# Performance work log

Hardware: AMD Instinct MI355X
Metric: run time of the kernel (lower is better)

The kernel has to match this reference:

```python
import jax, jax.numpy as jnp
import numpy as np

DIM = 512

def setup_inputs() -> dict:
    key = jax.random.key(0)
    ks = jax.random.split(key, 10)
    B, N, D = 8, 4096, DIM
    s = 1.0 / np.sqrt(D)
    return {
        "x": jax.random.normal(ks[0], (B, N, D), dtype=jnp.float32),
        "wq": jax.random.normal(ks[1], (D, D), dtype=jnp.float32) * s,
        "bq": jnp.zeros((D,), dtype=jnp.float32),
        "wk": jax.random.normal(ks[2], (D, D), dtype=jnp.float32) * s,
        "bk": jnp.zeros((D,), dtype=jnp.float32),
        "wp": jax.random.normal(ks[3], (D, D), dtype=jnp.float32) * s,
        "bp": jnp.zeros((D,), dtype=jnp.float32),
        "wf": jax.random.normal(ks[4], (D, D), dtype=jnp.float32) * s,
        "bf": jnp.zeros((D,), dtype=jnp.float32),
        "w_g": jax.random.normal(ks[5], (D, 1), dtype=jnp.float32),
    }

def reference(x, wq, bq, wk, bk, wp, bp, wf, bf, w_g):
    D = x.shape[-1]
    scale = D ** (-0.5)
    query = x @ wq + bq                      # [B,N,D]
    key_t = x @ wk + bk                      # [B,N,D]
    # l2 normalize along last dim (tf.math.l2_normalize uses eps=1e-12 via rsqrt of max(sum_sq, eps))
    def l2n(t):
        ss = jnp.sum(t * t, axis=-1, keepdims=True)
        return t * jax.lax.rsqrt(jnp.maximum(ss, 1e-12))
    query = l2n(query)
    key_t = l2n(key_t)
    query_weight = query @ w_g               # [B,N,1]
    scaled = query_weight * scale
    # Faithful to TF code: softmax over axis=-1 of a size-1 axis -> all ones
    attn = jax.nn.softmax(scaled, axis=-1)   # [B,N,1] == 1.0
    global_queries = jnp.sum(attn * query, axis=1)  # [B,D]
    gq = global_queries[:, None, :]          # broadcast over N (tile)
    out = (gq * key_t) @ wp + bp + query     # [B,N,D]
    out = out @ wf + bf
    return out
```

## Files before the change

### kernel.cpp

```cpp
#include <hip/hip_runtime.h>
#include <stdint.h>

typedef __bf16 bf16x8 __attribute__((ext_vector_type(8)));
typedef float floatx4 __attribute__((ext_vector_type(4)));
typedef unsigned short u16;
typedef u16 u16x8 __attribute__((ext_vector_type(8)));

__device__ __forceinline__ float bf2f(u16 u) {
    union { uint32_t i; float f; } v; v.i = ((uint32_t)u) << 16; return v.f;
}
__device__ __forceinline__ u16 f2bf(float f) {
    union { float f; uint32_t i; } v; v.f = f;
    uint32_t r = v.i + 0x7fffu + ((v.i >> 16) & 1u);
    return (u16)(r >> 16);
}

__device__ __forceinline__ void gload_lds16(const u16* g, u16* l) {
    __builtin_amdgcn_global_load_lds(
        (const __attribute__((address_space(1))) void*)g,
        (__attribute__((address_space(3))) void*)l,
        16, 0, 0);
}

#define BK 64
template<int EPI>
__global__ __launch_bounds__(512, 2) void gemm_bt(
    const u16* __restrict__ A, int lda,
    const u16* __restrict__ Bt, long bstride,
    const float* __restrict__ bias,
    const u16* __restrict__ addsrc, int ldadd,
    const float* __restrict__ ssq_add,
    const float* __restrict__ ssq_row,
    float* __restrict__ ssq_out,
    u16* __restrict__ C16, float* __restrict__ C32, int ldc,
    int K)
{
    __shared__ __attribute__((aligned(16))) u16 lds[2 * 32768];
    const int tid  = threadIdx.x;
    const int wave = tid >> 6;
    const int lane = tid & 63;
    const int quad = lane >> 4;
    const int l16  = lane & 15;
    const int wm = wave >> 2, wn = wave & 3;

    const int gx   = gridDim.x;
    const int nwg  = gx * gridDim.y;
    const int wgid = blockIdx.y * gx + blockIdx.x;
    const int cpx  = nwg >> 3;
    const int swz  = (wgid & 7) * cpx + (wgid >> 3);
    const int row0 = (swz / gx) * 256;
    const int col0 = (swz % gx) * 256;
    const int batch = row0 >> 12;
    const int Mtot  = gridDim.y * 256;

    floatx4 acc[8][4] = {};

    const int rsub = lane >> 3;
    const int ksub = ((lane & 7) ^ rsub) << 3;
    const u16* aptr[4]; const u16* bptr[4];
    const u16* Bb = Bt + (size_t)batch * bstride;
#pragma unroll
    for (int c = 0; c < 4; ++c) {
        const int cc = wave * 4 + c;
        aptr[c] = A  + (size_t)(row0 + cc * 8 + rsub) * lda + ksub;
        bptr[c] = Bb + (size_t)(col0 + cc * 8 + rsub) * K   + ksub;
    }

    const int NT = K >> 6;

#define STAGE(T, B)                                                        \
    {                                                                      \
        u16* sA_ = &lds[(B) * 32768];                                      \
        u16* sB_ = sA_ + 16384;                                            \
        const int kt_ = (T) * BK;                                          \
        _Pragma("unroll")                                                  \
        for (int c = 0; c < 4; ++c) {                                      \
            const int cc = wave * 4 + c;                                   \
            gload_lds16(aptr[c] + kt_, &sA_[cc * 512]);                    \
            gload_lds16(bptr[c] + kt_, &sB_[cc * 512]);                    \
        }                                                                  \
    }

    STAGE(0, 0);
    STAGE(1, 1);

    for (int t = 0; t < NT; ++t) {
        if (t + 1 < NT) asm volatile("s_waitcnt vmcnt(8)" ::: "memory");
        else            asm volatile("s_waitcnt vmcnt(0)" ::: "memory");
        __builtin_amdgcn_s_barrier();
        __builtin_amdgcn_sched_barrier(0);

        const u16* sA = &lds[(t & 1) * 32768];
        const u16* sB = sA + 16384;
#pragma unroll
        for (int ks = 0; ks < 2; ++ks) {
            const int cidx = ks * 4 + quad;
            const int pgo = ((cidx ^ (l16 & 7)) << 3);
            bf16x8 bfr[4];
#pragma unroll
            for (int n = 0; n < 4; ++n)
                bfr[n] = *(const bf16x8*)&sB[(wn * 64 + n * 16 + l16) * BK + pgo];
            __builtin_amdgcn_s_setprio(1);
#pragma unroll
            for (int m = 0; m < 8; ++m) {
                bf16x8 af = *(const bf16x8*)&sA[(wm * 128 + m * 16 + l16) * BK + pgo];
#pragma unroll
                for (int n = 0; n < 4; ++n)
                    acc[m][n] = __builtin_amdgcn_mfma_f32_16x16x32_bf16(af, bfr[n], acc[m][n], 0, 0, 0);
            }
            __builtin_amdgcn_s_setprio(0);
        }

        __builtin_amdgcn_sched_barrier(0);
        asm volatile("" ::: "memory");
        __builtin_amdgcn_s_barrier();
        asm volatile("" ::: "memory");
        if (t + 2 < NT) STAGE(t + 2, t & 1);
    }
#undef STAGE

    if constexpr (EPI == 0 || EPI == 1) {
        u16* til = lds;
#pragma unroll
        for (int h = 0; h < 2; ++h) {
            __syncthreads();
            if (wm == h) {
                float bv[4];
#pragma unroll
                for (int n = 0; n < 4; ++n) bv[n] = bias[col0 + wn * 64 + n * 16 + l16];
#pragma unroll
                for (int m = 0; m < 8; ++m) {
                    int rowl = m * 16 + quad * 4;
                    int rowb = row0 + h * 128 + rowl;
                    float rsr4[4], rsa4[4];
                    if constexpr (EPI == 1) {
                        float4 rr = *(const float4*)&ssq_row[rowb];
                        float4 ra = *(const float4*)&ssq_add[rowb];
                        rsr4[0] = rsqrtf(fmaxf(rr.x, 1e-12f));
                        rsr4[1] = rsqrtf(fmaxf(rr.y, 1e-12f));
                        rsr4[2] = rsqrtf(fmaxf(rr.z, 1e-12f));
                        rsr4[3] = rsqrtf(fmaxf(rr.w, 1e-12f));
                        rsa4[0] = rsqrtf(fmaxf(ra.x, 1e-12f));
                        rsa4[1] = rsqrtf(fmaxf(ra.y, 1e-12f));
                        rsa4[2] = rsqrtf(fmaxf(ra.z, 1e-12f));
                        rsa4[3] = rsqrtf(fmaxf(ra.w, 1e-12f));
                    }
#pragma unroll
                    for (int n = 0; n < 4; ++n) {
                        int tcol = wn * 64 + n * 16 + l16;
#pragma unroll
                        for (int t = 0; t < 4; ++t) {
                            float v;
                            if constexpr (EPI == 1) {
                                v = acc[m][n][t] * rsr4[t] + bv[n]
                                  + bf2f(addsrc[(size_t)(rowb + t) * ldadd + col0 + tcol]) * rsa4[t];
                            } else {
                                v = acc[m][n][t] + bv[n];
                            }
                            til[(rowl + t) * 264 + tcol] = f2bf(v);
                        }
                    }
                }
            }
            __syncthreads();
            float ssl[8];
#pragma unroll
            for (int c = 0; c < 8; ++c) {
                int r  = c * 16 + (tid >> 5);
                int cu = (tid & 31) * 8;
                ushort4 lo = *(const ushort4*)&til[r * 264 + cu];
                ushort4 hi = *(const ushort4*)&til[r * 264 + cu + 4];
                u16x8 o;
                o[0] = lo.x; o[1] = lo.y; o[2] = lo.z; o[3] = lo.w;
                o[4] = hi.x; o[5] = hi.y; o[6] = hi.z; o[7] = hi.w;
                *(u16x8*)&C16[(size_t)(row0 + h * 128 + r) * ldc + col0 + cu] = o;
                if constexpr (EPI == 0) {
                    float ss = 0.f;
#pragma unroll
                    for (int q2 = 0; q2 < 8; ++q2) { float f = bf2f(o[q2]); ss += f * f; }
                    ssl[c] = ss;
                }
            }
            if constexpr (EPI == 0) {
                float* so = ssq_out + (size_t)(col0 >> 9) * Mtot + row0 + h * 128;
#pragma unroll
                for (int c = 0; c < 8; ++c) {
                    float s = ssl[c];
                    s += __shfl_xor(s, 1);
                    s += __shfl_xor(s, 2);
                    s += __shfl_xor(s, 4);
                    s += __shfl_xor(s, 8);
                    s += __shfl_xor(s, 16);
                    if ((lane & 31) == 0) atomicAdd(&so[c * 16 + (tid >> 5)], s);
                }
            }
        }
    } else {
        float* ftile = (float*)lds;
#pragma unroll
        for (int p = 0; p < 4; ++p) {
            __syncthreads();
            if (wm == (p >> 1)) {
                float bv[4];
#pragma unroll
                for (int n = 0; n < 4; ++n) bv[n] = bias[col0 + wn * 64 + n * 16 + l16];
#pragma unroll
                for (int mi = 0; mi < 4; ++mi) {
                    int m = (p & 1) * 4 + mi;
                    int rowl = mi * 16 + quad * 4;
#pragma unroll
                    for (int n = 0; n < 4; ++n) {
                        int tcol = wn * 64 + n * 16 + l16;
#pragma unroll
                        for (int t = 0; t < 4; ++t)
                            ftile[(rowl + t) * 264 + tcol] = acc[m][n][t] + bv[n];
                    }
                }
            }
            __syncthreads();
#pragma unroll
            for (int c = 0; c < 8; ++c) {
                int r  = c * 8 + wave;
                int cu = lane * 4;
                float4 v = *(const float4*)&ftile[r * 264 + cu];
                *(float4*)&C32[(size_t)(row0 + p * 64 + r) * ldc + col0 + cu] = v;
            }
        }
    }
}

__global__ __launch_bounds__(256) void gsum_kernel(const u16* __restrict__ QK,
                                                   const float* __restrict__ ssqQ,
                                                   float* __restrict__ g)
{
    __shared__ float gtile[4][512];
    const int lane = threadIdx.x & 63;
    const int wave = threadIdx.x >> 6;
    const int row0 = blockIdx.x * 128 + wave * 32;
    const int batch = row0 >> 12;
    const int d = lane * 8;
    float gacc[8] = {};
    for (int rr = 0; rr < 32; ++rr) {
        int row = row0 + rr;
        float s = rsqrtf(fmaxf(ssqQ[row], 1e-12f));
        u16x8 q = *(const u16x8*)(QK + (size_t)row * 1024 + d);
#pragma unroll
        for (int i = 0; i < 8; ++i) gacc[i] += s * bf2f(q[i]);
    }
#pragma unroll
    for (int i = 0; i < 8; ++i) gtile[wave][d + i] = gacc[i];
    __syncthreads();
    int c2 = threadIdx.x * 2;
    float s0 = gtile[0][c2]     + gtile[1][c2]     + gtile[2][c2]     + gtile[3][c2];
    float s1 = gtile[0][c2 + 1] + gtile[1][c2 + 1] + gtile[2][c2 + 1] + gtile[3][c2 + 1];
    atomicAdd(&g[batch * 512 + c2], s0);
    atomicAdd(&g[batch * 512 + c2 + 1], s1);
}

__global__ __launch_bounds__(256) void scale_wp_kernel(const float* __restrict__ wp,
                                                       const float* __restrict__ g,
                                                       u16* __restrict__ BtP8)
{
    __shared__ u16 tile[32][34];
    const int b   = blockIdx.x >> 8;
    const int bid = blockIdx.x & 255;
    const int tk = bid & 15;
    const int tn = bid >> 4;
    const int c  = threadIdx.x & 31;
    const int r0 = threadIdx.x >> 5;
    const float* gb = g + b * 512;
#pragma unroll
    for (int i = 0; i < 4; ++i) {
        int r = r0 + i * 8;
        int k = tk * 32 + r;
        tile[r][c] = f2bf(gb[k] * wp[(size_t)k * 512 + tn * 32 + c]);
    }
    __syncthreads();
    u16* Bt = BtP8 + (size_t)b * 512 * 512;
#pragma unroll
    for (int i = 0; i < 4; ++i) {
        int r = r0 + i * 8;
        Bt[(size_t)(tn * 32 + r) * 512 + tk * 32 + c] = tile[c][r];
    }
}

__global__ __launch_bounds__(256) void convert_x_kernel(const float* __restrict__ x, u16* __restrict__ xb)
{
    size_t i = ((size_t)blockIdx.x * 256 + threadIdx.x) * 4;
    float4 v = *(const float4*)(x + i);
    ushort4 o;
    o.x = f2bf(v.x); o.y = f2bf(v.y); o.z = f2bf(v.z); o.w = f2bf(v.w);
    *(ushort4*)(xb + i) = o;
}

__global__ __launch_bounds__(256) void transpose3_kernel(
    const float* __restrict__ w0, const float* __restrict__ w1, const float* __restrict__ w2,
    u16* __restrict__ d0, u16* __restrict__ d1, u16* __restrict__ d2)
{
    __shared__ u16 tile[32][34];
    const int which = blockIdx.x >> 8;
    const float* W = (which == 0) ? w0 : (which == 1) ? w1 : w2;
    u16* Bt = (which == 0) ? d0 : (which == 1) ? d1 : d2;
    const int bid = blockIdx.x & 255;
    const int tk = bid & 15;
    const int tn = bid >> 4;
    const int c  = threadIdx.x & 31;
    const int r0 = threadIdx.x >> 5;
#pragma unroll
    for (int i = 0; i < 4; ++i) {
        int r = r0 + i * 8;
        tile[r][c] = f2bf(W[(size_t)(tk * 32 + r) * 512 + tn * 32 + c]);
    }
    __syncthreads();
#pragma unroll
    for (int i = 0; i < 4; ++i) {
        int r = r0 + i * 8;
        Bt[(size_t)(tn * 32 + r) * 512 + tk * 32 + c] = tile[c][r];
    }
}

__global__ __launch_bounds__(256) void setup_kernel(const float* __restrict__ bq,
                                                    const float* __restrict__ bk,
                                                    float* __restrict__ biasQK,
                                                    float* __restrict__ g,
                                                    float* __restrict__ ssq)
{
    int id = blockIdx.x * 256 + threadIdx.x;
    if (id < 1024) biasQK[id] = (id < 512) ? bq[id] : bk[id - 512];
    if (id < 4096) g[id] = 0.f;
    ssq[id] = 0.f;
}

extern "C" void kernel_launch(void* const* d_in, const int* in_sizes, int n_in,
                              void* d_out, int out_size, void* d_ws, size_t ws_size,
                              hipStream_t stream)
{
    const float* x  = (const float*)d_in[0];
    const float* wq = (const float*)d_in[1];
    const float* bq = (const float*)d_in[2];
    const float* wk = (const float*)d_in[3];
    const float* bk = (const float*)d_in[4];
    const float* wp = (const float*)d_in[5];
    const float* bp = (const float*)d_in[6];
    const float* wf = (const float*)d_in[7];
    const float* bf = (const float*)d_in[8];

    char* ws = (char*)d_ws;
    u16*   xb     = (u16*)(ws);
    u16*   T      = (u16*)(ws);
    u16*   QK     = (u16*)(ws + 33554432);
    u16*   Bt1    = (u16*)(ws + 100663296);
    u16*   BtP8   = (u16*)(ws + 101711872);
    u16*   BtF    = (u16*)(ws + 105906176);
    float* biasQK = (float*)(ws + 106430464);
    float* g      = (float*)(ws + 106434560);
    float* ssq    = (float*)(ws + 106450944);

    setup_kernel<<<256, 256, 0, stream>>>(bq, bk, biasQK, g, ssq);
    convert_x_kernel<<<16384, 256, 0, stream>>>(x, xb);
    transpose3_kernel<<<768, 256, 0, stream>>>(wq, wk, wf, Bt1, Bt1 + 512 * 512, BtF);

    gemm_bt<0><<<dim3(4, 128), 512, 0, stream>>>(
        xb, 512, Bt1, 0, biasQK, nullptr, 0, nullptr, nullptr, ssq, QK, nullptr, 1024, 512);
    gsum_kernel<<<256, 256, 0, stream>>>(QK, ssq, g);
    scale_wp_kernel<<<2048, 256, 0, stream>>>(wp, g, BtP8);
    gemm_bt<1><<<dim3(2, 128), 512, 0, stream>>>(
        QK + 512, 1024, BtP8, 512 * 512, bp, QK, 1024, ssq, ssq + 32768, nullptr, T, nullptr, 512, 512);
    gemm_bt<2><<<dim3(2, 128), 512, 0, stream>>>(
        T, 512, BtF, 0, bf, nullptr, 0, nullptr, nullptr, nullptr, nullptr, (float*)d_out, 512, 512);
}
```

Baseline: 254.8 us.

## Restructure GEMM main loop into four barrier-synchronized MFMA sub-phases with single-stage prefetch

The mainloop is rewritten so each K-tile is computed in four quadrant sub-phases. Each wave loads a quarter of its A/B fragments from LDS, synchronizes with a workgroup barrier, then issues a batch of MFMAs at raised priority, which staggers LDS reads and matrix work across waves. Global-to-LDS staging now prefetches one tile ahead instead of two, and the staging layout is regrouped by half-tile rows. The added barriers per tile and the shallower prefetch trade latency hiding for tighter inter-wave scheduling.

Result: no change. 257.3 us (+1.0%).

```diff
diff --git a/kernel.cpp b/kernel.cpp
--- a/kernel.cpp
+++ b/kernel.cpp
@@ -57,65 +57,133 @@
 
     const int rsub = lane >> 3;
     const int ksub = ((lane & 7) ^ rsub) << 3;
-    const u16* aptr[4]; const u16* bptr[4];
     const u16* Bb = Bt + (size_t)batch * bstride;
-#pragma unroll
-    for (int c = 0; c < 4; ++c) {
-        const int cc = wave * 4 + c;
-        aptr[c] = A  + (size_t)(row0 + cc * 8 + rsub) * lda + ksub;
-        bptr[c] = Bb + (size_t)(col0 + cc * 8 + rsub) * K   + ksub;
-    }
+    const u16* aP = A  + (size_t)(row0 + wave * 8 + rsub) * lda + ksub;
+    const u16* bP = Bb + (size_t)(col0 + wave * 8 + rsub) * K   + ksub;
 
     const int NT = K >> 6;
 
-#define STAGE(T, B)                                                        \
-    {                                                                      \
-        u16* sA_ = &lds[(B) * 32768];                                      \
-        u16* sB_ = sA_ + 16384;                                            \
-        const int kt_ = (T) * BK;                                          \
-        _Pragma("unroll")                                                  \
-        for (int c = 0; c < 4; ++c) {                                      \
-            const int cc = wave * 4 + c;                                   \
-            gload_lds16(aptr[c] + kt_, &sA_[cc * 512]);                    \
-            gload_lds16(bptr[c] + kt_, &sB_[cc * 512]);                    \
-        }                                                                  \
-    }
-
-    STAGE(0, 0);
-    STAGE(1, 1);
+#define STAGE(T)                                                              \
+    {                                                                         \
+        u16* dst_ = &lds[((T) & 1) * 32768];                                  \
+        const int kt_ = (T) * BK;                                             \
+        _Pragma("unroll")                                                     \
+        for (int h_ = 0; h_ < 2; ++h_)                                        \
+        { _Pragma("unroll")                                                   \
+          for (int j_ = 0; j_ < 2; ++j_) {                                    \
+            gload_lds16(aP + (size_t)(h_ * 128 + j_ * 64) * lda + kt_,        \
+                        dst_ + h_ * 8192 + j_ * 4096 + wave * 512);           \
+            gload_lds16(bP + (size_t)(h_ * 128 + j_ * 64) * K + kt_,          \
+                        dst_ + 16384 + h_ * 8192 + j_ * 4096 + wave * 512);   \
+          } }                                                                 \
+    }
+
+    STAGE(0);
+    asm volatile("s_waitcnt vmcnt(0)" ::: "memory");
+    __builtin_amdgcn_s_barrier();
 
     for (int t = 0; t < NT; ++t) {
-        if (t + 1 < NT) asm volatile("s_waitcnt vmcnt(8)" ::: "memory");
-        else            asm volatile("s_waitcnt vmcnt(0)" ::: "memory");
-        __builtin_amdgcn_s_barrier();
-        __builtin_amdgcn_sched_barrier(0);
-
-        const u16* sA = &lds[(t & 1) * 32768];
-        const u16* sB = sA + 16384;
-#pragma unroll
-        for (int ks = 0; ks < 2; ++ks) {
-            const int cidx = ks * 4 + quad;
-            const int pgo = ((cidx ^ (l16 & 7)) << 3);
-            bf16x8 bfr[4];
-#pragma unroll
-            for (int n = 0; n < 4; ++n)
-                bfr[n] = *(const bf16x8*)&sB[(wn * 64 + n * 16 + l16) * BK + pgo];
-            __builtin_amdgcn_s_setprio(1);
-#pragma unroll
-            for (int m = 0; m < 8; ++m) {
-                bf16x8 af = *(const bf16x8*)&sA[(wm * 128 + m * 16 + l16) * BK + pgo];
-#pragma unroll
-                for (int n = 0; n < 4; ++n)
-                    acc[m][n] = __builtin_amdgcn_mfma_f32_16x16x32_bf16(af, bfr[n], acc[m][n], 0, 0, 0);
-            }
-            __builtin_amdgcn_s_setprio(0);
-        }
-
-        __builtin_amdgcn_sched_barrier(0);
-        asm volatile("" ::: "memory");
-        __builtin_amdgcn_s_barrier();
-        asm volatile("" ::: "memory");
-        if (t + 2 < NT) STAGE(t + 2, t & 1);
+        const u16* buf = &lds[(t & 1) * 32768];
+        const u16* sA = buf + wm * 8192;
+        const u16* sB = buf + 16384 + (wn >> 1) * 8192;
+        const int brl = (wn & 1) * 64;
+        bf16x8 af[4][2], bb[2][2];
+
+#pragma unroll
+        for (int m = 0; m < 4; ++m)
+#pragma unroll
+            for (int ks = 0; ks < 2; ++ks)
+                af[m][ks] = *(const bf16x8*)&sA[(m * 16 + l16) * 64 + (((ks * 4 + quad) ^ (l16 & 7)) << 3)];
+#pragma unroll
+        for (int n = 0; n < 2; ++n)
+#pragma unroll
+            for (int ks = 0; ks < 2; ++ks)
+                bb[n][ks] = *(const bf16x8*)&sB[(brl + n * 16 + l16) * 64 + (((ks * 4 + quad) ^ (l16 & 7)) << 3)];
+        if (t + 1 < NT) STAGE(t + 1);
+        __builtin_amdgcn_sched_barrier(0);
+        __builtin_amdgcn_s_barrier();
+        asm volatile("s_waitcnt lgkmcnt(0)" ::: "memory");
+        __builtin_amdgcn_sched_barrier(0);
+        __builtin_amdgcn_s_setprio(1);
+#pragma unroll
+        for (int ks = 0; ks < 2; ++ks)
+#pragma unroll
+            for (int m = 0; m < 4; ++m)
+#pragma unroll
+                for (int n = 0; n < 2; ++n)
+                    acc[m][n] = __builtin_amdgcn_mfma_f32_16x16x32_bf16(af[m][ks], bb[n][ks], acc[m][n], 0, 0, 0);
+        __builtin_amdgcn_s_setprio(0);
+        __builtin_amdgcn_sched_barrier(0);
+        __builtin_amdgcn_s_barrier();
+
+#pragma unroll
+        for (int n = 0; n < 2; ++n)
+#pragma unroll
+            for (int ks = 0; ks < 2; ++ks)
+                bb[n][ks] = *(const bf16x8*)&sB[(brl + (n + 2) * 16 + l16) * 64 + (((ks * 4 + quad) ^ (l16 & 7)) << 3)];
+        __builtin_amdgcn_sched_barrier(0);
+        __builtin_amdgcn_s_barrier();
+        asm volatile("s_waitcnt lgkmcnt(0)" ::: "memory");
+        __builtin_amdgcn_sched_barrier(0);
+        __builtin_amdgcn_s_setprio(1);
+#pragma unroll
+        for (int ks = 0; ks < 2; ++ks)
+#pragma unroll
+            for (int m = 0; m < 4; ++m)
+#pragma unroll
+                for (int n = 0; n < 2; ++n)
+                    acc[m][n + 2] = __builtin_amdgcn_mfma_f32_16x16x32_bf16(af[m][ks], bb[n][ks], acc[m][n + 2], 0, 0, 0);
+        __builtin_amdgcn_s_setprio(0);
+        __builtin_amdgcn_sched_barrier(0);
+        __builtin_amdgcn_s_barrier();
+
+#pragma unroll
+        for (int m = 0; m < 4; ++m)
+#pragma unroll
+            for (int ks = 0; ks < 2; ++ks)
+                af[m][ks] = *(const bf16x8*)&sA[((m + 4) * 16 + l16) * 64 + (((ks * 4 + quad) ^ (l16 & 7)) << 3)];
+#pragma unroll
+        for (int n = 0; n < 2; ++n)
+#pragma unroll
+            for (int ks = 0; ks < 2; ++ks)
+                bb[n][ks] = *(const bf16x8*)&sB[(brl + n * 16 + l16) * 64 + (((ks * 4 + quad) ^ (l16 & 7)) << 3)];
+        __builtin_amdgcn_sched_barrier(0);
+        __builtin_amdgcn_s_barrier();
+        asm volatile("s_waitcnt lgkmcnt(0)" ::: "memory");
+        __builtin_amdgcn_sched_barrier(0);
+        __builtin_amdgcn_s_setprio(1);
+#pragma unroll
+        for (int ks = 0; ks < 2; ++ks)
+#pragma unroll
+            for (int m = 0; m < 4; ++m)
+#pragma unroll
+                for (int n = 0; n < 2; ++n)
+                    acc[m + 4][n] = __builtin_amdgcn_mfma_f32_16x16x32_bf16(af[m][ks], bb[n][ks], acc[m + 4][n], 0, 0, 0);
+        __builtin_amdgcn_s_setprio(0);
+        __builtin_amdgcn_sched_barrier(0);
+        __builtin_amdgcn_s_barrier();
+
+#pragma unroll
+        for (int n = 0; n < 2; ++n)
+#pragma unroll
+            for (int ks = 0; ks < 2; ++ks)
+                bb[n][ks] = *(const bf16x8*)&sB[(brl + (n + 2) * 16 + l16) * 64 + (((ks * 4 + quad) ^ (l16 & 7)) << 3)];
+        __builtin_amdgcn_sched_barrier(0);
+        __builtin_amdgcn_s_barrier();
+        asm volatile("s_waitcnt lgkmcnt(0)" ::: "memory");
+        __builtin_amdgcn_sched_barrier(0);
+        __builtin_amdgcn_s_setprio(1);
+#pragma unroll
+        for (int ks = 0; ks < 2; ++ks)
+#pragma unroll
+            for (int m = 0; m < 4; ++m)
+#pragma unroll
+                for (int n = 0; n < 2; ++n)
+                    acc[m + 4][n + 2] = __builtin_amdgcn_mfma_f32_16x16x32_bf16(af[m][ks], bb[n][ks], acc[m + 4][n + 2], 0, 0, 0);
+        __builtin_amdgcn_s_setprio(0);
+        __builtin_amdgcn_sched_barrier(0);
+        if (t + 1 < NT) asm volatile("s_waitcnt vmcnt(0)" ::: "memory");
+        __builtin_amdgcn_s_barrier();
     }
 #undef STAGE
 
```

## Fold projection and final GEMMs into one K=1024 GEMM via precomputed Wp·Wf

Applied to the files above, without the earlier changes.

Precomputes Wp@Wf (transposed, bf16) and the combined bias bp@Wf+bf once, then scales it per batch by the global query vector. The last two chained GEMMs become a single GEMM over the concatenated [query|key] activations (K=1024). The query half is rescaled mid-loop by the ratio of the two norm factors so a single key-norm scale can be applied in the epilogue. This removes the intermediate T round trip and one full 32K×512 GEMM pass, at the cost of extra small setup kernels and a different bf16 rounding order.

Result: no change. 256.0 us (+0.5%).

```diff
diff --git a/kernel.cpp b/kernel.cpp
--- a/kernel.cpp
+++ b/kernel.cpp
@@ -23,17 +23,149 @@
 }
 
 #define BK 64
-template<int EPI>
-__global__ __launch_bounds__(512, 2) void gemm_bt(
-    const u16* __restrict__ A, int lda,
-    const u16* __restrict__ Bt, long bstride,
+
+__global__ __launch_bounds__(512, 2) void gemm1_kernel(
+    const u16* __restrict__ A,
+    const u16* __restrict__ Bt,
     const float* __restrict__ bias,
-    const u16* __restrict__ addsrc, int ldadd,
-    const float* __restrict__ ssq_add,
-    const float* __restrict__ ssq_row,
     float* __restrict__ ssq_out,
-    u16* __restrict__ C16, float* __restrict__ C32, int ldc,
-    int K)
+    u16* __restrict__ C16)
+{
+    __shared__ __attribute__((aligned(16))) u16 lds[2 * 32768];
+    const int tid  = threadIdx.x;
+    const int wave = tid >> 6;
+    const int lane = tid & 63;
+    const int quad = lane >> 4;
+    const int l16  = lane & 15;
+    const int wm = wave >> 2, wn = wave & 3;
+
+    const int gx   = gridDim.x;
+    const int nwg  = gx * gridDim.y;
+    const int wgid = blockIdx.y * gx + blockIdx.x;
+    const int cpx  = nwg >> 3;
+    const int swz  = (wgid & 7) * cpx + (wgid >> 3);
+    const int row0 = (swz / gx) * 256;
+    const int col0 = (swz % gx) * 256;
+
+    floatx4 acc[8][4] = {};
+
+    const int rsub = lane >> 3;
+    const int ksub = ((lane & 7) ^ rsub) << 3;
+    const u16* aptr[4]; const u16* bptr[4];
+#pragma unroll
+    for (int c = 0; c < 4; ++c) {
+        const int cc = wave * 4 + c;
+        aptr[c] = A  + (size_t)(row0 + cc * 8 + rsub) * 512 + ksub;
+        bptr[c] = Bt + (size_t)(col0 + cc * 8 + rsub) * 512 + ksub;
+    }
+    const int NT = 8;
+
+#define STAGE1(T, B)                                                          \
+    {                                                                         \
+        u16* dA_ = &lds[(B) * 32768];                                         \
+        u16* dB_ = dA_ + 16384;                                               \
+        const int kt_ = (T) * BK;                                             \
+        _Pragma("unroll")                                                     \
+        for (int c = 0; c < 4; ++c) {                                         \
+            const int cc = wave * 4 + c;                                      \
+            gload_lds16(aptr[c] + kt_, dA_ + cc * 512);                       \
+            gload_lds16(bptr[c] + kt_, dB_ + cc * 512);                       \
+        }                                                                     \
+    }
+
+    STAGE1(0, 0);
+    STAGE1(1, 1);
+    for (int t = 0; t < NT; ++t) {
+        if (t + 1 < NT) asm volatile("s_waitcnt vmcnt(8)" ::: "memory");
+        else            asm volatile("s_waitcnt vmcnt(0)" ::: "memory");
+        __builtin_amdgcn_s_barrier();
+        __builtin_amdgcn_sched_barrier(0);
+        const u16* sA = &lds[(t & 1) * 32768];
+        const u16* sB = sA + 16384;
+#pragma unroll
+        for (int ks = 0; ks < 2; ++ks) {
+            const int pgo = (((ks * 4 + quad) ^ (l16 & 7)) << 3);
+            bf16x8 bfr[4];
+#pragma unroll
+            for (int n = 0; n < 4; ++n)
+                bfr[n] = *(const bf16x8*)&sB[(wn * 64 + n * 16 + l16) * 64 + pgo];
+            __builtin_amdgcn_s_setprio(1);
+#pragma unroll
+            for (int m = 0; m < 8; ++m) {
+                bf16x8 af = *(const bf16x8*)&sA[(wm * 128 + m * 16 + l16) * 64 + pgo];
+#pragma unroll
+                for (int n = 0; n < 4; ++n)
+                    acc[m][n] = __builtin_amdgcn_mfma_f32_16x16x32_bf16(af, bfr[n], acc[m][n], 0, 0, 0);
+            }
+            __builtin_amdgcn_s_setprio(0);
+        }
+        __builtin_amdgcn_sched_barrier(0);
+        asm volatile("" ::: "memory");
+        __builtin_amdgcn_s_barrier();
+        asm volatile("" ::: "memory");
+        if (t + 2 < NT) STAGE1(t + 2, t & 1);
+    }
+#undef STAGE1
+
+    u16* til = lds;
+#pragma unroll
+    for (int h = 0; h < 2; ++h) {
+        __syncthreads();
+        if (wm == h) {
+            float bv[4];
+#pragma unroll
+            for (int n = 0; n < 4; ++n) bv[n] = bias[col0 + wn * 64 + n * 16 + l16];
+#pragma unroll
+            for (int m = 0; m < 8; ++m) {
+                int rowl = m * 16 + quad * 4;
+#pragma unroll
+                for (int n = 0; n < 4; ++n) {
+                    int tcol = wn * 64 + n * 16 + l16;
+#pragma unroll
+                    for (int t = 0; t < 4; ++t)
+                        til[(rowl + t) * 264 + tcol] = f2bf(acc[m][n][t] + bv[n]);
+                }
+            }
+        }
+        __syncthreads();
+        float ssl[8];
+#pragma unroll
+        for (int c = 0; c < 8; ++c) {
+            int r  = c * 16 + (tid >> 5);
+            int cu = (tid & 31) * 8;
+            ushort4 lo = *(const ushort4*)&til[r * 264 + cu];
+            ushort4 hi = *(const ushort4*)&til[r * 264 + cu + 4];
+            u16x8 o;
+            o[0] = lo.x; o[1] = lo.y; o[2] = lo.z; o[3] = lo.w;
+            o[4] = hi.x; o[5] = hi.y; o[6] = hi.z; o[7] = hi.w;
+            *(u16x8*)&C16[(size_t)(row0 + h * 128 + r) * 1024 + col0 + cu] = o;
+            float ss = 0.f;
+#pragma unroll
+            for (int q2 = 0; q2 < 8; ++q2) { float f = bf2f(o[q2]); ss += f * f; }
+            ssl[c] = ss;
+        }
+        float* so = ssq_out + (size_t)(col0 >> 9) * 32768 + row0 + h * 128;
+#pragma unroll
+        for (int c = 0; c < 8; ++c) {
+            float s = ssl[c];
+            s += __shfl_xor(s, 1);
+            s += __shfl_xor(s, 2);
+            s += __shfl_xor(s, 4);
+            s += __shfl_xor(s, 8);
+            s += __shfl_xor(s, 16);
+            if ((lane & 31) == 0) atomicAdd(&so[c * 16 + (tid >> 5)], s);
+        }
+    }
+}
+
+__global__ __launch_bounds__(512, 2) void gemm_qk_kernel(
+    const u16* __restrict__ A,
+    const u16* __restrict__ BtF,
+    const u16* __restrict__ BtPF,
+    const float* __restrict__ bpf,
+    const float* __restrict__ ssqQ,
+    const float* __restrict__ ssqK,
+    float* __restrict__ C32)
 {
     __shared__ __attribute__((aligned(16))) u16 lds[2 * 32768];
     const int tid  = threadIdx.x;
@@ -51,181 +183,209 @@
     const int row0 = (swz / gx) * 256;
     const int col0 = (swz % gx) * 256;
     const int batch = row0 >> 12;
-    const int Mtot  = gridDim.y * 256;
 
     floatx4 acc[8][4] = {};
 
     const int rsub = lane >> 3;
     const int ksub = ((lane & 7) ^ rsub) << 3;
-    const u16* aptr[4]; const u16* bptr[4];
-    const u16* Bb = Bt + (size_t)batch * bstride;
+    const u16* aptr[4]; const u16* bptrF[4]; const u16* bptrP[4];
+    const u16* BP = BtPF + (size_t)batch * 262144;
 #pragma unroll
     for (int c = 0; c < 4; ++c) {
         const int cc = wave * 4 + c;
-        aptr[c] = A  + (size_t)(row0 + cc * 8 + rsub) * lda + ksub;
-        bptr[c] = Bb + (size_t)(col0 + cc * 8 + rsub) * K   + ksub;
-    }
-
-    const int NT = K >> 6;
-
-#define STAGE(T, B)                                                        \
-    {                                                                      \
-        u16* sA_ = &lds[(B) * 32768];                                      \
-        u16* sB_ = sA_ + 16384;                                            \
-        const int kt_ = (T) * BK;                                          \
-        _Pragma("unroll")                                                  \
-        for (int c = 0; c < 4; ++c) {                                      \
-            const int cc = wave * 4 + c;                                   \
-            gload_lds16(aptr[c] + kt_, &sA_[cc * 512]);                    \
-            gload_lds16(bptr[c] + kt_, &sB_[cc * 512]);                    \
-        }                                                                  \
-    }
-
-    STAGE(0, 0);
-    STAGE(1, 1);
-
+        aptr[c]  = A   + (size_t)(row0 + cc * 8 + rsub) * 1024 + ksub;
+        bptrF[c] = BtF + (size_t)(col0 + cc * 8 + rsub) * 512  + ksub;
+        bptrP[c] = BP  + (size_t)(col0 + cc * 8 + rsub) * 512  + ksub;
+    }
+    const int NT = 16;
+
+#define STAGEQ(T, B)                                                          \
+    {                                                                         \
+        u16* dA_ = &lds[(B) * 32768];                                         \
+        u16* dB_ = dA_ + 16384;                                               \
+        const int kt_ = (T) * BK;                                             \
+        _Pragma("unroll")                                                     \
+        for (int c = 0; c < 4; ++c) {                                         \
+            const int cc = wave * 4 + c;                                      \
+            gload_lds16(aptr[c] + kt_, dA_ + cc * 512);                       \
+            const u16* bsrc_ = (kt_ < 512) ? (bptrF[c] + kt_)                 \
+                                           : (bptrP[c] + (kt_ - 512));        \
+            gload_lds16(bsrc_, dB_ + cc * 512);                               \
+        }                                                                     \
+    }
+
+    STAGEQ(0, 0);
+    STAGEQ(1, 1);
     for (int t = 0; t < NT; ++t) {
         if (t + 1 < NT) asm volatile("s_waitcnt vmcnt(8)" ::: "memory");
         else            asm volatile("s_waitcnt vmcnt(0)" ::: "memory");
         __builtin_amdgcn_s_barrier();
         __builtin_amdgcn_sched_barrier(0);
-
         const u16* sA = &lds[(t & 1) * 32768];
         const u16* sB = sA + 16384;
 #pragma unroll
         for (int ks = 0; ks < 2; ++ks) {
-            const int cidx = ks * 4 + quad;
-            const int pgo = ((cidx ^ (l16 & 7)) << 3);
+            const int pgo = (((ks * 4 + quad) ^ (l16 & 7)) << 3);
             bf16x8 bfr[4];
 #pragma unroll
             for (int n = 0; n < 4; ++n)
-                bfr[n] = *(const bf16x8*)&sB[(wn * 64 + n * 16 + l16) * BK + pgo];
+                bfr[n] = *(const bf16x8*)&sB[(wn * 64 + n * 16 + l16) * 64 + pgo];
             __builtin_amdgcn_s_setprio(1);
 #pragma unroll
             for (int m = 0; m < 8; ++m) {
-                bf16x8 af = *(const bf16x8*)&sA[(wm * 128 + m * 16 + l16) * BK + pgo];
+                bf16x8 af = *(const bf16x8*)&sA[(wm * 128 + m * 16 + l16) * 64 + pgo];
 #pragma unroll
                 for (int n = 0; n < 4; ++n)
                     acc[m][n] = __builtin_amdgcn_mfma_f32_16x16x32_bf16(af, bfr[n], acc[m][n], 0, 0, 0);
             }
             __builtin_amdgcn_s_setprio(0);
         }
-
+        if (t == 7) {
+#pragma unroll
+            for (int m = 0; m < 8; ++m) {
+                int rowb = row0 + wm * 128 + m * 16 + quad * 4;
+                float4 q4 = *(const float4*)&ssqQ[rowb];
+                float4 k4 = *(const float4*)&ssqK[rowb];
+                float ratio[4];
+                ratio[0] = rsqrtf(fmaxf(q4.x, 1e-12f)) / rsqrtf(fmaxf(k4.x, 1e-12f));
+                ratio[1] = rsqrtf(fmaxf(q4.y, 1e-12f)) / rsqrtf(fmaxf(k4.y, 1e-12f));
+                ratio[2] = rsqrtf(fmaxf(q4.z, 1e-12f)) / rsqrtf(fmaxf(k4.z, 1e-12f));
+                ratio[3] = rsqrtf(fmaxf(q4.w, 1e-12f)) / rsqrtf(fmaxf(k4.w, 1e-12f));
+#pragma unroll
+                for (int n = 0; n < 4; ++n)
+#pragma unroll
+                    for (int tt = 0; tt < 4; ++tt)
+                        acc[m][n][tt] *= ratio[tt];
+            }
+        }
         __builtin_amdgcn_sched_barrier(0);
         asm volatile("" ::: "memory");
         __builtin_amdgcn_s_barrier();
         asm volatile("" ::: "memory");
-        if (t + 2 < NT) STAGE(t + 2, t & 1);
-    }
-#undef STAGE
-
-    if constexpr (EPI == 0 || EPI == 1) {
-        u16* til = lds;
-#pragma unroll
-        for (int h = 0; h < 2; ++h) {
-            __syncthreads();
-            if (wm == h) {
-                float bv[4];
-#pragma unroll
-                for (int n = 0; n < 4; ++n) bv[n] = bias[col0 + wn * 64 + n * 16 + l16];
-#pragma unroll
-                for (int m = 0; m < 8; ++m) {
-                    int rowl = m * 16 + quad * 4;
-                    int rowb = row0 + h * 128 + rowl;
-                    float rsr4[4], rsa4[4];
-                    if constexpr (EPI == 1) {
-                        float4 rr = *(const float4*)&ssq_row[rowb];
-                        float4 ra = *(const float4*)&ssq_add[rowb];
-                        rsr4[0] = rsqrtf(fmaxf(rr.x, 1e-12f));
-                        rsr4[1] = rsqrtf(fmaxf(rr.y, 1e-12f));
-                        rsr4[2] = rsqrtf(fmaxf(rr.z, 1e-12f));
-                        rsr4[3] = rsqrtf(fmaxf(rr.w, 1e-12f));
-                        rsa4[0] = rsqrtf(fmaxf(ra.x, 1e-12f));
-                        rsa4[1] = rsqrtf(fmaxf(ra.y, 1e-12f));
-                        rsa4[2] = rsqrtf(fmaxf(ra.z, 1e-12f));
-                        rsa4[3] = rsqrtf(fmaxf(ra.w, 1e-12f));
-                    }
-#pragma unroll
-                    for (int n = 0; n < 4; ++n) {
-                        int tcol = wn * 64 + n * 16 + l16;
-#pragma unroll
-                        for (int t = 0; t < 4; ++t) {
-                            float v;
-                            if constexpr (EPI == 1) {
-                                v = acc[m][n][t] * rsr4[t] + bv[n]
-                                  + bf2f(addsrc[(size_t)(rowb + t) * ldadd + col0 + tcol]) * rsa4[t];
-                            } else {
-                                v = acc[m][n][t] + bv[n];
-                            }
-                            til[(rowl + t) * 264 + tcol] = f2bf(v);
-                        }
-                    }
+        if (t + 2 < NT) STAGEQ(t + 2, t & 1);
+    }
+#undef STAGEQ
+
+    float* ftile = (float*)lds;
+#pragma unroll
+    for (int p = 0; p < 4; ++p) {
+        __syncthreads();
+        if (wm == (p >> 1)) {
+            float bv[4];
+#pragma unroll
+            for (int n = 0; n < 4; ++n) bv[n] = bpf[col0 + wn * 64 + n * 16 + l16];
+#pragma unroll
+            for (int mi = 0; mi < 4; ++mi) {
+                int m = (p & 1) * 4 + mi;
+                int rowl = mi * 16 + quad * 4;
+                int rowb = row0 + p * 64 + rowl;
+                float4 k4 = *(const float4*)&ssqK[rowb];
+                float rsk4[4];
+                rsk4[0] = rsqrtf(fmaxf(k4.x, 1e-12f));
+                rsk4[1] = rsqrtf(fmaxf(k4.y, 1e-12f));
+                rsk4[2] = rsqrtf(fmaxf(k4.z, 1e-12f));
+                rsk4[3] = rsqrtf(fmaxf(k4.w, 1e-12f));
+#pragma unroll
+                for (int n = 0; n < 4; ++n) {
+                    int tcol = wn * 64 + n * 16 + l16;
+#pragma unroll
+                    for (int t = 0; t < 4; ++t)
+                        ftile[(rowl + t) * 264 + tcol] = acc[m][n][t] * rsk4[t] + bv[n];
                 }
             }
-            __syncthreads();
-            float ssl[8];
-#pragma unroll
-            for (int c = 0; c < 8; ++c) {
-                int r  = c * 16 + (tid >> 5);
-                int cu = (tid & 31) * 8;
-                ushort4 lo = *(const ushort4*)&til[r * 264 + cu];
-                ushort4 hi = *(const ushort4*)&til[r * 264 + cu + 4];
-                u16x8 o;
-                o[0] = lo.x; o[1] = lo.y; o[2] = lo.z; o[3] = lo.w;
-                o[4] = hi.x; o[5] = hi.y; o[6] = hi.z; o[7] = hi.w;
-                *(u16x8*)&C16[(size_t)(row0 + h * 128 + r) * ldc + col0 + cu] = o;
-                if constexpr (EPI == 0) {
-                    float ss = 0.f;
-#pragma unroll
-                    for (int q2 = 0; q2 < 8; ++q2) { float f = bf2f(o[q2]); ss += f * f; }
-                    ssl[c] = ss;
-                }
-            }
-            if constexpr (EPI == 0) {
-                float* so = ssq_out + (size_t)(col0 >> 9) * Mtot + row0 + h * 128;
-#pragma unroll
-                for (int c = 0; c < 8; ++c) {
-                    float s = ssl[c];
-                    s += __shfl_xor(s, 1);
-                    s += __shfl_xor(s, 2);
-                    s += __shfl_xor(s, 4);
-                    s += __shfl_xor(s, 8);
-                    s += __shfl_xor(s, 16);
-                    if ((lane & 31) == 0) atomicAdd(&so[c * 16 + (tid >> 5)], s);
-                }
-            }
-        }
-    } else {
-        float* ftile = (float*)lds;
-#pragma unroll
-        for (int p = 0; p < 4; ++p) {
-            __syncthreads();
-            if (wm == (p >> 1)) {
-                float bv[4];
-#pragma unroll
-                for (int n = 0; n < 4; ++n) bv[n] = bias[col0 + wn * 64 + n * 16 + l16];
-#pragma unroll
-                for (int mi = 0; mi < 4; ++mi) {
-                    int m = (p & 1) * 4 + mi;
-                    int rowl = mi * 16 + quad * 4;
-#pragma unroll
-                    for (int n = 0; n < 4; ++n) {
-                        int tcol = wn * 64 + n * 16 + l16;
-#pragma unroll
-                        for (int t = 0; t < 4; ++t)
-                            ftile[(rowl + t) * 264 + tcol] = acc[m][n][t] + bv[n];
-                    }
-                }
-            }
-            __syncthreads();
-#pragma unroll
-            for (int c = 0; c < 8; ++c) {
-                int r  = c * 8 + wave;
-                int cu = lane * 4;
-                float4 v = *(const float4*)&ftile[r * 264 + cu];
-                *(float4*)&C32[(size_t)(row0 + p * 64 + r) * ldc + col0 + cu] = v;
-            }
-        }
+        }
+        __syncthreads();
+#pragma unroll
+        for (int c = 0; c < 8; ++c) {
+            int r  = c * 8 + wave;
+            int cu = lane * 4;
+            float4 v = *(const float4*)&ftile[r * 264 + cu];
+            *(float4*)&C32[(size_t)(row0 + p * 64 + r) * 512 + col0 + cu] = v;
+        }
+    }
+}
+
+__global__ __launch_bounds__(256) void gemm128_kernel(
+    const u16* __restrict__ A, int lda,
+    const u16* __restrict__ Bt, int ldb,
+    u16* __restrict__ C16, int ldc, int K)
+{
+    __shared__ __attribute__((aligned(16))) u16 lds[128 * 132];
+    u16* lsA = lds;
+    u16* lsB = lds + 128 * BK;
+    const int tid  = threadIdx.x;
+    const int wave = tid >> 6;
+    const int lane = tid & 63;
+    const int quad = lane >> 4;
+    const int l16  = lane & 15;
+    const int wm = wave >> 1, wn = wave & 1;
+
+    const int gx   = gridDim.x;
+    const int nwg  = gx * gridDim.y;
+    const int wgid = blockIdx.y * gx + blockIdx.x;
+    const int cpx  = nwg >> 3;
+    const int swz  = (wgid & 7) * cpx + (wgid >> 3);
+    const int row0 = (swz / gx) * 128;
+    const int col0 = (swz % gx) * 128;
+
+    floatx4 acc[4][4] = {};
+    const int rsub = lane >> 3;
+    const int ksub = ((lane & 7) ^ rsub) << 3;
+    const u16* aptr[4]; const u16* bptr[4];
+#pragma unroll
+    for (int c = 0; c < 4; ++c) {
+        const int cc = wave * 4 + c;
+        aptr[c] = A  + (size_t)(row0 + cc * 8 + rsub) * lda + ksub;
+        bptr[c] = Bt + (size_t)(col0 + cc * 8 + rsub) * ldb + ksub;
+    }
+    for (int kt = 0; kt < K; kt += BK) {
+#pragma unroll
+        for (int c = 0; c < 4; ++c) {
+            const int cc = wave * 4 + c;
+            gload_lds16(aptr[c] + kt, &lsA[cc * 512]);
+            gload_lds16(bptr[c] + kt, &lsB[cc * 512]);
+        }
+        __syncthreads();
+#pragma unroll
+        for (int ks = 0; ks < 2; ++ks) {
+            const int pgo = (((ks * 4 + quad) ^ (l16 & 7)) << 3);
+            bf16x8 af[4], bfr[4];
+#pragma unroll
+            for (int i = 0; i < 4; ++i)
+                af[i] = *(const bf16x8*)&lsA[(wm * 64 + i * 16 + l16) * BK + pgo];
+#pragma unroll
+            for (int j = 0; j < 4; ++j)
+                bfr[j] = *(const bf16x8*)&lsB[(wn * 64 + j * 16 + l16) * BK + pgo];
+#pragma unroll
+            for (int i = 0; i < 4; ++i)
+#pragma unroll
+                for (int j = 0; j < 4; ++j)
+                    acc[i][j] = __builtin_amdgcn_mfma_f32_16x16x32_bf16(af[i], bfr[j], acc[i][j], 0, 0, 0);
+        }
+        __syncthreads();
+    }
+#pragma unroll
+    for (int j = 0; j < 4; ++j) {
+        int tcol = wn * 64 + j * 16 + l16;
+#pragma unroll
+        for (int i = 0; i < 4; ++i) {
+            int trow = wm * 64 + i * 16 + quad * 4;
+#pragma unroll
+            for (int t = 0; t < 4; ++t)
+                lds[(trow + t) * 132 + tcol] = f2bf(acc[i][j][t]);
+        }
+    }
+    __syncthreads();
+#pragma unroll
+    for (int c = 0; c < 8; ++c) {
+        int r  = c * 16 + (tid >> 4);
+        int cu = (tid & 15) * 8;
+        ushort4 lo = *(const ushort4*)&lds[r * 132 + cu];
+        ushort4 hi = *(const ushort4*)&lds[r * 132 + cu + 4];
+        u16x8 o;
+        o[0] = lo.x; o[1] = lo.y; o[2] = lo.z; o[3] = lo.w;
+        o[4] = hi.x; o[5] = hi.y; o[6] = hi.z; o[7] = hi.w;
+        *(u16x8*)&C16[(size_t)(row0 + r) * ldc + col0 + cu] = o;
     }
 }
 
@@ -257,31 +417,37 @@
     atomicAdd(&g[batch * 512 + c2 + 1], s1);
 }
 
-__global__ __launch_bounds__(256) void scale_wp_kernel(const float* __restrict__ wp,
-                                                       const float* __restrict__ g,
-                                                       u16* __restrict__ BtP8)
-{
-    __shared__ u16 tile[32][34];
-    const int b   = blockIdx.x >> 8;
-    const int bid = blockIdx.x & 255;
-    const int tk = bid & 15;
-    const int tn = bid >> 4;
-    const int c  = threadIdx.x & 31;
-    const int r0 = threadIdx.x >> 5;
-    const float* gb = g + b * 512;
-#pragma unroll
-    for (int i = 0; i < 4; ++i) {
-        int r = r0 + i * 8;
-        int k = tk * 32 + r;
-        tile[r][c] = f2bf(gb[k] * wp[(size_t)k * 512 + tn * 32 + c]);
-    }
-    __syncthreads();
-    u16* Bt = BtP8 + (size_t)b * 512 * 512;
-#pragma unroll
-    for (int i = 0; i < 4; ++i) {
-        int r = r0 + i * 8;
-        Bt[(size_t)(tn * 32 + r) * 512 + tk * 32 + c] = tile[c][r];
-    }
+__global__ __launch_bounds__(256) void scalePF_kernel(const u16* __restrict__ Pt,
+                                                      const float* __restrict__ g,
+                                                      u16* __restrict__ BtPF)
+{
+    size_t i8 = ((size_t)blockIdx.x * 256 + threadIdx.x) * 8;
+    int b   = (int)(i8 >> 18);
+    int rem = (int)(i8 & 262143);
+    int kk  = rem & 511;
+    u16x8 p = *(const u16x8*)(Pt + rem);
+    float4 g0 = *(const float4*)(g + b * 512 + kk);
+    float4 g1 = *(const float4*)(g + b * 512 + kk + 4);
+    u16x8 o;
+    o[0] = f2bf(bf2f(p[0]) * g0.x); o[1] = f2bf(bf2f(p[1]) * g0.y);
+    o[2] = f2bf(bf2f(p[2]) * g0.z); o[3] = f2bf(bf2f(p[3]) * g0.w);
+    o[4] = f2bf(bf2f(p[4]) * g1.x); o[5] = f2bf(bf2f(p[5]) * g1.y);
+    o[6] = f2bf(bf2f(p[6]) * g1.z); o[7] = f2bf(bf2f(p[7]) * g1.w);
+    *(u16x8*)(BtPF + (size_t)b * 262144 + rem) = o;
+}
+
+__global__ __launch_bounds__(512) void bpf_kernel(const float* __restrict__ wf,
+                                                  const float* __restrict__ bp,
+                                                  const float* __restrict__ bfv,
+                                                  float* __restrict__ bpf)
+{
+    int n = threadIdx.x;
+    int j0 = blockIdx.x * 64;
+    float s = 0.f;
+#pragma unroll 8
+    for (int j = j0; j < j0 + 64; ++j) s += bp[j] * wf[(size_t)j * 512 + n];
+    if (blockIdx.x == 0) s += bfv[n];
+    atomicAdd(&bpf[n], s);
 }
 
 __global__ __launch_bounds__(256) void convert_x_kernel(const float* __restrict__ x, u16* __restrict__ xb)
@@ -291,6 +457,15 @@
     ushort4 o;
     o.x = f2bf(v.x); o.y = f2bf(v.y); o.z = f2bf(v.z); o.w = f2bf(v.w);
     *(ushort4*)(xb + i) = o;
+}
+
+__global__ __launch_bounds__(256) void convert_wp_kernel(const float* __restrict__ wp, u16* __restrict__ wpb)
+{
+    size_t i = ((size_t)blockIdx.x * 256 + threadIdx.x) * 4;
+    float4 v = *(const float4*)(wp + i);
+    ushort4 o;
+    o.x = f2bf(v.x); o.y = f2bf(v.y); o.z = f2bf(v.z); o.w = f2bf(v.w);
+    *(ushort4*)(wpb + i) = o;
 }
 
 __global__ __launch_bounds__(256) void transpose3_kernel(
@@ -323,11 +498,13 @@
                                                     const float* __restrict__ bk,
                                                     float* __restrict__ biasQK,
                                                     float* __restrict__ g,
-                                                    float* __restrict__ ssq)
+                                                    float* __restrict__ ssq,
+                                                    float* __restrict__ bpf)
 {
     int id = blockIdx.x * 256 + threadIdx.x;
     if (id < 1024) biasQK[id] = (id < 512) ? bq[id] : bk[id - 512];
     if (id < 4096) g[id] = 0.f;
+    if (id < 512)  bpf[id] = 0.f;
     ssq[id] = 0.f;
 }
 
@@ -347,25 +524,26 @@
 
     char* ws = (char*)d_ws;
     u16*   xb     = (u16*)(ws);
-    u16*   T      = (u16*)(ws);
     u16*   QK     = (u16*)(ws + 33554432);
     u16*   Bt1    = (u16*)(ws + 100663296);
-    u16*   BtP8   = (u16*)(ws + 101711872);
-    u16*   BtF    = (u16*)(ws + 105906176);
-    float* biasQK = (float*)(ws + 106430464);
-    float* g      = (float*)(ws + 106434560);
-    float* ssq    = (float*)(ws + 106450944);
-
-    setup_kernel<<<256, 256, 0, stream>>>(bq, bk, biasQK, g, ssq);
+    u16*   BtF    = (u16*)(ws + 101711872);
+    u16*   wpb    = (u16*)(ws + 102236160);
+    u16*   Pt     = (u16*)(ws + 102760448);
+    u16*   BtPF   = (u16*)(ws + 103284736);
+    float* biasQK = (float*)(ws + 107479040);
+    float* g      = (float*)(ws + 107483136);
+    float* ssq    = (float*)(ws + 107499520);
+    float* bpf    = (float*)(ws + 107761664);
+
+    setup_kernel<<<256, 256, 0, stream>>>(bq, bk, biasQK, g, ssq, bpf);
     convert_x_kernel<<<16384, 256, 0, stream>>>(x, xb);
     transpose3_kernel<<<768, 256, 0, stream>>>(wq, wk, wf, Bt1, Bt1 + 512 * 512, BtF);
-
-    gemm_bt<0><<<dim3(4, 128), 512, 0, stream>>>(
-        xb, 512, Bt1, 0, biasQK, nullptr, 0, nullptr, nullptr, ssq, QK, nullptr, 1024, 512);
+    convert_wp_kernel<<<256, 256, 0, stream>>>(wp, wpb);
+    bpf_kernel<<<8, 512, 0, stream>>>(wf, bp, bf, bpf);
+    gemm128_kernel<<<dim3(4, 4), 256, 0, stream>>>(BtF, 512, wpb, 512, Pt, 512, 512);
+
+    gemm1_kernel<<<dim3(4, 128), 512, 0, stream>>>(xb, Bt1, biasQK, ssq, QK);
     gsum_kernel<<<256, 256, 0, stream>>>(QK, ssq, g);
-    scale_wp_kernel<<<2048, 256, 0, stream>>>(wp, g, BtP8);
-    gemm_bt<1><<<dim3(2, 128), 512, 0, stream>>>(
-        QK + 512, 1024, BtP8, 512 * 512, bp, QK, 1024, ssq, ssq + 32768, nullptr, T, nullptr, 512, 512);
-    gemm_bt<2><<<dim3(2, 128), 512, 0, stream>>>(
-        T, 512, BtF, 0, bf, nullptr, 0, nullptr, nullptr, nullptr, nullptr, (float*)d_out, 512, 512);
-}
+    scalePF_kernel<<<1024, 256, 0, stream>>>(Pt, g, BtPF);
+    gemm_qk_kernel<<<dim3(2, 128), 512, 0, stream>>>(QK, BtF, BtPF, bpf, ssq, ssq + 32768, (float*)d_out);
+}
```
